# Optimization experiments

Hardware: AMD Instinct MI355X
Metric: run time of the kernel (lower is better)

## Reference

```python
import jax, jax.numpy as jnp
import numpy as np
from jax import lax

# TT-conv configuration (matches init_kwargs)
M = (4, 8, 8)        # in_c_modes, prod = 256
O = (4, 8, 8)        # out_c_modes, prod = 256
R = (16, 16, 16, 1)  # ranks with trailing 1 appended as in the module
B, H, W = 8, 64, 64
IN_C = int(np.prod(M))


def setup_inputs() -> dict:
    key = jax.random.key(0)
    ks = jax.random.split(key, 6)
    X = jax.random.normal(ks[0], (B, IN_C, H, W), jnp.float32)
    conv_w = jax.random.normal(ks[1], (R[0], 1, 3, 3), jnp.float32) * 0.3
    conv_b = jax.random.normal(ks[2], (R[0],), jnp.float32) * 0.05
    def xavier(k, shape):
        fan_in, fan_out = shape[1], shape[0]
        std = (2.0 / (fan_in + fan_out)) ** 0.5
        return jax.random.normal(k, shape, jnp.float32) * std
    core1 = xavier(ks[3], (O[0] * R[1], R[0] * M[0]))  # (64, 64)
    core2 = xavier(ks[4], (O[1] * R[2], R[1] * M[1]))  # (128, 128)
    core3 = xavier(ks[5], (O[2] * R[3], R[2] * M[2]))  # (8, 128)
    return {"X": X, "conv_w": conv_w, "conv_b": conv_b,
            "core1": core1, "core2": core2, "core3": core3}


def reference(X, conv_w, conv_b, core1, core2, core3):
    b, in_c, h, w = X.shape
    # core0: depth-agnostic 1->r0 conv applied per input channel
    y = lax.conv_general_dilated(
        X.reshape(-1, 1, h, w), conv_w,
        window_strides=(1, 1), padding=((1, 1), (1, 1)),
        dimension_numbers=("NCHW", "OIHW", "NCHW"))
    y = y + conv_b[None, :, None, None]          # (B*in_c, r0, h, w)
    hh, ww = y.shape[-2:]
    # (B, m1, m2, m3, r0, h, w): in_c factored row-major, m1 most significant
    y = y.reshape(b, M[0], M[1], M[2], R[0], hh, ww)
    # TT cores reshaped (o_i, r_{i+1}, r_i, m_i)
    G1 = core1.reshape(O[0], R[1], R[0], M[0])
    G2 = core2.reshape(O[1], R[2], R[1], M[1])
    G3 = core3.reshape(O[2], R[3], R[2], M[2])
    # Full TT contraction chain collapsed into one einsum; s (=r3) has size 1.
    out = jnp.einsum("bijkrhw,auri,cvuj,dsvk->bacdhw",
                     y, G1, G2, G3, optimize=True)
    # channel order (o1, o2, o3) with o3 fastest, as in the torch module
    return out.reshape(b, O[0] * O[1] * O[2], hh, ww)
```

## Files before the change

kernel.cpp:

```cpp
#include <hip/hip_runtime.h>
#include <hip/hip_bf16.h>
#include <stdint.h>

typedef __attribute__((ext_vector_type(8))) short short8;
typedef __attribute__((ext_vector_type(4))) float f32x4;

#define XP_BYTES   17842176
#define XP_PAD     1024
#define OFF_W9     (XP_BYTES + XP_PAD)
#define W9_BYTES   (8*9*256*32*2)
#define OFF_BIAS   (OFF_W9 + W9_BYTES)

__device__ __forceinline__ short f2bf(float f) {
  __hip_bfloat16 h = __float2bfloat16(f);
  return *reinterpret_cast<short*>(&h);
}

__device__ __forceinline__ void gl_lds16(const void* g, void* l) {
  __builtin_amdgcn_global_load_lds(
      (const __attribute__((address_space(1))) void*)g,
      (__attribute__((address_space(3))) void*)l, 16, 0, 0);
}

__global__ void k_weights(const float* __restrict__ core1,
                          const float* __restrict__ core2,
                          const float* __restrict__ core3,
                          const float* __restrict__ convw,
                          const float* __restrict__ convb,
                          short* __restrict__ W9, float* __restrict__ bias) {
  __shared__ float H2s[1024];
  __shared__ float red[256];
  const int o = blockIdx.x, c = threadIdx.x;
  const int a = o >> 6, c2 = (o >> 3) & 7, d = o & 7;
#pragma unroll
  for (int p = 0; p < 4; ++p) {
    int idx = c + (p << 8);
    int k = idx & 7, j = (idx >> 3) & 7, u = idx >> 6;
    float s = 0.f;
#pragma unroll
    for (int v = 0; v < 16; ++v)
      s += core2[(c2 * 16 + v) * 128 + u * 8 + j] * core3[d * 128 + v * 8 + k];
    H2s[idx] = s;
  }
  __syncthreads();
  const int i = c >> 6, j = (c >> 3) & 7, k = c & 7;
  float Wr[16];
#pragma unroll
  for (int r = 0; r < 16; ++r) Wr[r] = 0.f;
  for (int u = 0; u < 16; ++u) {
    float h = H2s[u * 64 + j * 8 + k];
    const float* c1 = core1 + (a * 16 + u) * 64 + i;
#pragma unroll
    for (int r = 0; r < 16; ++r) Wr[r] += c1[r * 4] * h;
  }
  const int cb = c >> 5, cl = c & 31, g = cl >> 3, pos = cl & 7;
  const int gslot = g ^ (o & 3);
#pragma unroll
  for (int t = 0; t < 9; ++t) {
    float s = 0.f;
#pragma unroll
    for (int r = 0; r < 16; ++r) s += Wr[r] * convw[r * 9 + t];
    W9[((size_t)((cb * 9 + t) * 256 + o)) * 32 + gslot * 8 + pos] = f2bf(s);
  }
  float s = 0.f;
#pragma unroll
  for (int r = 0; r < 16; ++r) s += Wr[r] * convb[r];
  red[c] = s;
  __syncthreads();
  for (int st = 128; st > 0; st >>= 1) {
    if (c < st) red[c] += red[c + st];
    __syncthreads();
  }
  if (c == 0) bias[o] = red[0];
}

__global__ void k_pad(const float* __restrict__ X, short* __restrict__ Xp) {
  const int yp = blockIdx.x, b = blockIdx.y, cb = blockIdx.z;
  const int t = threadIdx.x;
  const int x = t & 63, sub = t >> 6;
  const size_t rowg = ((size_t)((b * 8 + cb) * 66 + yp)) * 264;
  const short8 z = (short8){0, 0, 0, 0, 0, 0, 0, 0};
  if (yp == 0 || yp == 65) {
    *(short8*)(Xp + (rowg + (size_t)(x << 2) + sub) * 8) = z;
    if (x < 2)
      *(short8*)(Xp + (rowg + (size_t)((64 + x) << 2) + sub) * 8) = z;
    return;
  }
  const int y = yp - 1, xp = x + 1;
  const int gslot = sub ^ (xp & 3);
  const float* src = X + ((size_t)(b * 256 + cb * 32 + sub * 8) * 64 + y) * 64 + x;
  short8 v;
#pragma unroll
  for (int k = 0; k < 8; ++k) v[k] = f2bf(src[(size_t)k * 4096]);
  *(short8*)(Xp + (rowg + (size_t)(xp << 2) + gslot) * 8) = v;
  if (x < 2)
    *(short8*)(Xp + (rowg + (size_t)((x * 65) << 2) + sub) * 8) = z;
}

__device__ __forceinline__ void stage_tiles(
    const short* __restrict__ Xp, const short* __restrict__ W9,
    short* XLd, short* WLd, int cb, int h0, int oBase, int b, int wv, int lane) {
  const size_t xb = ((size_t)(((b << 3) + cb) * 66 + h0) * 66) << 5;
#pragma unroll 1
  for (int q = wv; q < 42; q += 4)
    gl_lds16(Xp + xb + (q << 9) + (lane << 3), XLd + (q << 9));
#pragma unroll 1
  for (int q = wv; q < 36; q += 4) {
    const int t = q >> 2, sub = q & 3;
    const short* g = W9 +
        (((size_t)(((cb * 9 + t) << 8) + oBase + (sub << 4))) << 5) + (lane << 3);
    gl_lds16(g, WLd + (((t << 6) + (sub << 4)) << 5));
  }
}

__global__ __launch_bounds__(256, 1) void k_gemm(
    const short* __restrict__ Xp, const short* __restrict__ W9,
    const float* __restrict__ bias, float* __restrict__ out) {
  __shared__ __align__(16) short XL[2][21504];
  __shared__ __align__(16) short WL[2][18432];

  const int tid  = threadIdx.x;
  const int lane = tid & 63;
  const int wv   = tid >> 6;
  const int l15  = lane & 15;
  const int gl   = lane >> 4;
  const int h0    = blockIdx.x << 3;
  const int oBase = blockIdx.y << 6;
  const int b     = blockIdx.z;
  const int r0    = wv << 1;

  f32x4 acc[2][4][4];
#pragma unroll
  for (int rr = 0; rr < 2; ++rr)
#pragma unroll
    for (int io = 0; io < 4; ++io)
#pragma unroll
      for (int ip = 0; ip < 4; ++ip)
        acc[rr][io][ip] = (f32x4){0.f, 0.f, 0.f, 0.f};

  stage_tiles(Xp, W9, &XL[0][0], &WL[0][0], 0, h0, oBase, b, wv, lane);

  int cur = 0;
  for (int cb = 0; cb < 8; ++cb) {
    __syncthreads();
    if (cb < 7)
      stage_tiles(Xp, W9, &XL[cur ^ 1][0], &WL[cur ^ 1][0],
                  cb + 1, h0, oBase, b, wv, lane);
    const short* XLc = &XL[cur][0];
    const short* WLc = &WL[cur][0];
#pragma unroll
    for (int dx = 0; dx < 3; ++dx) {
      short8 bfr[4][4];
#pragma unroll
      for (int xr = 0; xr < 4; ++xr) {
        const int prow = r0 + xr;
#pragma unroll
        for (int ip = 0; ip < 4; ++ip) {
          const int x = (ip << 4) + l15 + dx;
          bfr[xr][ip] = *(const short8*)&XLc[(((prow * 66 + x) << 2) + (gl ^ (x & 3))) << 3];
        }
      }
#pragma unroll
      for (int dy = 0; dy < 3; ++dy) {
        const int t = dy * 3 + dx;
        short8 af[4];
#pragma unroll
        for (int io = 0; io < 4; ++io) {
          const int ol = (io << 4) + l15;
          af[io] = *(const short8*)&WLc[(((t << 6) + ol) << 5) + ((gl ^ (ol & 3)) << 3)];
        }
#pragma unroll
        for (int io = 0; io < 4; ++io)
#pragma unroll
          for (int ip = 0; ip < 4; ++ip) {
            acc[0][io][ip] = __builtin_amdgcn_mfma_f32_16x16x32_bf16(
                af[io], bfr[dy][ip], acc[0][io][ip], 0, 0, 0);
            acc[1][io][ip] = __builtin_amdgcn_mfma_f32_16x16x32_bf16(
                af[io], bfr[dy + 1][ip], acc[1][io][ip], 0, 0, 0);
          }
      }
    }
    cur ^= 1;
  }

#pragma unroll
  for (int rr = 0; rr < 2; ++rr) {
    const int h = h0 + r0 + rr;
#pragma unroll
    for (int io = 0; io < 4; ++io) {
#pragma unroll
      for (int r = 0; r < 4; ++r) {
        const int oG = oBase + (io << 4) + (gl << 2) + r;
        const float bv = bias[oG];
        float* op = out + (((size_t)((b << 8) + oG)) << 12) + (h << 6);
#pragma unroll
        for (int ip = 0; ip < 4; ++ip)
          op[(ip << 4) + l15] = acc[rr][io][ip][r] + bv;
      }
    }
  }
}

extern "C" void kernel_launch(void* const* d_in, const int* in_sizes, int n_in,
                              void* d_out, int out_size, void* d_ws, size_t ws_size,
                              hipStream_t stream) {
  (void)in_sizes; (void)n_in; (void)out_size; (void)ws_size;
  const float* X     = (const float*)d_in[0];
  const float* convw = (const float*)d_in[1];
  const float* convb = (const float*)d_in[2];
  const float* core1 = (const float*)d_in[3];
  const float* core2 = (const float*)d_in[4];
  const float* core3 = (const float*)d_in[5];
  float* out = (float*)d_out;
  char*  ws  = (char*)d_ws;

  short* Xp   = (short*)ws;
  short* W9   = (short*)(ws + OFF_W9);
  float* bias = (float*)(ws + OFF_BIAS);

  k_weights<<<256, 256, 0, stream>>>(core1, core2, core3, convw, convb, W9, bias);
  k_pad    <<<dim3(66, 8, 8), 256, 0, stream>>>(X, Xp);
  k_gemm   <<<dim3(8, 4, 8), 256, 0, stream>>>(Xp, W9, bias, out);
}
```

Baseline: 138.6 us.

## Halve output-channel tile, load weights from global, drop LDS double buffering

After: 138.8 us. No clear change (+0.2%).

```diff
diff --git a/kernel.cpp b/kernel.cpp
--- a/kernel.cpp
+++ b/kernel.cpp
@@ -87,7 +87,7 @@
     return;
   }
   const int y = yp - 1, xp = x + 1;
-  const int gslot = sub ^ (xp & 3);
+  const int gslot = sub ^ ((xp >> 1) & 3);
   const float* src = X + ((size_t)(b * 256 + cb * 32 + sub * 8) * 64 + y) * 64 + x;
   short8 v;
 #pragma unroll
@@ -97,27 +97,10 @@
     *(short8*)(Xp + (rowg + (size_t)((x * 65) << 2) + sub) * 8) = z;
 }
 
-__device__ __forceinline__ void stage_tiles(
-    const short* __restrict__ Xp, const short* __restrict__ W9,
-    short* XLd, short* WLd, int cb, int h0, int oBase, int b, int wv, int lane) {
-  const size_t xb = ((size_t)(((b << 3) + cb) * 66 + h0) * 66) << 5;
-#pragma unroll 1
-  for (int q = wv; q < 42; q += 4)
-    gl_lds16(Xp + xb + (q << 9) + (lane << 3), XLd + (q << 9));
-#pragma unroll 1
-  for (int q = wv; q < 36; q += 4) {
-    const int t = q >> 2, sub = q & 3;
-    const short* g = W9 +
-        (((size_t)(((cb * 9 + t) << 8) + oBase + (sub << 4))) << 5) + (lane << 3);
-    gl_lds16(g, WLd + (((t << 6) + (sub << 4)) << 5));
-  }
-}
-
-__global__ __launch_bounds__(256, 1) void k_gemm(
+__global__ __launch_bounds__(256, 2) void k_gemm(
     const short* __restrict__ Xp, const short* __restrict__ W9,
     const float* __restrict__ bias, float* __restrict__ out) {
-  __shared__ __align__(16) short XL[2][21504];
-  __shared__ __align__(16) short WL[2][18432];
+  __shared__ __align__(16) short XL[21504];
 
   const int tid  = threadIdx.x;
   const int lane = tid & 63;
@@ -125,31 +108,40 @@
   const int l15  = lane & 15;
   const int gl   = lane >> 4;
   const int h0    = blockIdx.x << 3;
-  const int oBase = blockIdx.y << 6;
+  const int oBase = blockIdx.y << 5;
   const int b     = blockIdx.z;
   const int r0    = wv << 1;
 
-  f32x4 acc[2][4][4];
+  f32x4 acc[2][2][4];
 #pragma unroll
   for (int rr = 0; rr < 2; ++rr)
 #pragma unroll
-    for (int io = 0; io < 4; ++io)
+    for (int io = 0; io < 2; ++io)
 #pragma unroll
       for (int ip = 0; ip < 4; ++ip)
         acc[rr][io][ip] = (f32x4){0.f, 0.f, 0.f, 0.f};
 
-  stage_tiles(Xp, W9, &XL[0][0], &WL[0][0], 0, h0, oBase, b, wv, lane);
-
-  int cur = 0;
   for (int cb = 0; cb < 8; ++cb) {
     __syncthreads();
-    if (cb < 7)
-      stage_tiles(Xp, W9, &XL[cur ^ 1][0], &WL[cur ^ 1][0],
-                  cb + 1, h0, oBase, b, wv, lane);
-    const short* XLc = &XL[cur][0];
-    const short* WLc = &WL[cur][0];
+    const size_t xb = ((size_t)(((b << 3) + cb) * 66 + h0) * 66) << 5;
+#pragma unroll 1
+    for (int q = wv; q < 42; q += 4)
+      gl_lds16(Xp + xb + (q << 9) + (lane << 3), &XL[q << 9]);
+    __syncthreads();
+
 #pragma unroll
     for (int dx = 0; dx < 3; ++dx) {
+      short8 af[3][2];
+#pragma unroll
+      for (int dy = 0; dy < 3; ++dy)
+#pragma unroll
+        for (int io = 0; io < 2; ++io) {
+          const int t = dy * 3 + dx;
+          const int ol = (io << 4) + l15;
+          af[dy][io] = *(const short8*)&W9[
+              (((size_t)((cb * 9 + t) * 256 + oBase + ol)) << 5) +
+              ((gl ^ (l15 & 3)) << 3)];
+        }
       short8 bfr[4][4];
 #pragma unroll
       for (int xr = 0; xr < 4; ++xr) {
@@ -157,37 +149,29 @@
 #pragma unroll
         for (int ip = 0; ip < 4; ++ip) {
           const int x = (ip << 4) + l15 + dx;
-          bfr[xr][ip] = *(const short8*)&XLc[(((prow * 66 + x) << 2) + (gl ^ (x & 3))) << 3];
+          bfr[xr][ip] = *(const short8*)&XL[
+              (((prow * 66 + x) << 2) + (gl ^ ((x >> 1) & 3))) << 3];
         }
       }
 #pragma unroll
-      for (int dy = 0; dy < 3; ++dy) {
-        const int t = dy * 3 + dx;
-        short8 af[4];
-#pragma unroll
-        for (int io = 0; io < 4; ++io) {
-          const int ol = (io << 4) + l15;
-          af[io] = *(const short8*)&WLc[(((t << 6) + ol) << 5) + ((gl ^ (ol & 3)) << 3)];
-        }
-#pragma unroll
-        for (int io = 0; io < 4; ++io)
+      for (int dy = 0; dy < 3; ++dy)
+#pragma unroll
+        for (int io = 0; io < 2; ++io)
 #pragma unroll
           for (int ip = 0; ip < 4; ++ip) {
             acc[0][io][ip] = __builtin_amdgcn_mfma_f32_16x16x32_bf16(
-                af[io], bfr[dy][ip], acc[0][io][ip], 0, 0, 0);
+                af[dy][io], bfr[dy][ip], acc[0][io][ip], 0, 0, 0);
             acc[1][io][ip] = __builtin_amdgcn_mfma_f32_16x16x32_bf16(
-                af[io], bfr[dy + 1][ip], acc[1][io][ip], 0, 0, 0);
+                af[dy][io], bfr[dy + 1][ip], acc[1][io][ip], 0, 0, 0);
           }
-      }
     }
-    cur ^= 1;
   }
 
 #pragma unroll
   for (int rr = 0; rr < 2; ++rr) {
     const int h = h0 + r0 + rr;
 #pragma unroll
-    for (int io = 0; io < 4; ++io) {
+    for (int io = 0; io < 2; ++io) {
 #pragma unroll
       for (int r = 0; r < 4; ++r) {
         const int oG = oBase + (io << 4) + (gl << 2) + r;
@@ -220,5 +204,5 @@
 
   k_weights<<<256, 256, 0, stream>>>(core1, core2, core3, convw, convb, W9, bias);
   k_pad    <<<dim3(66, 8, 8), 256, 0, stream>>>(X, Xp);
-  k_gemm   <<<dim3(8, 4, 8), 256, 0, stream>>>(Xp, W9, bias, out);
-}
+  k_gemm   <<<dim3(8, 8, 8), 256, 0, stream>>>(Xp, W9, bias, out);
+}
```
